# Kernel optimization log

Measured on AMD Instinct MI355X. Metric: run time of the kernel, lower is better.

Reference implementation:

```python
import jax, jax.numpy as jnp
import numpy as np

N = 50000
E = 800000


def _gcn_norm(edge_index, n):
    # Add self-loops and compute symmetric normalization coefficients per edge.
    src, dst = edge_index[0], edge_index[1]
    loop = jnp.arange(n, dtype=src.dtype)
    src = jnp.concatenate([src, loop])
    dst = jnp.concatenate([dst, loop])
    deg = jax.ops.segment_sum(jnp.ones_like(dst, dtype=jnp.float32), dst, num_segments=n)
    dis = jnp.where(deg > 0, 1.0 / jnp.sqrt(deg), 0.0)  # deg^-1/2
    norm = dis[src] * dis[dst]  # [E+N]
    return src, dst, norm


def _gcn_conv(x, W, b, src, dst, norm, n):
    h = x @ W                       # [N, F_out] dense transform first (PyG order)
    msg = h[src] * norm[:, None]    # gather + edgewise scale
    out = jax.ops.segment_sum(msg, dst, num_segments=n)  # scatter-add aggregate
    return out + b


def setup_inputs() -> dict:
    key = jax.random.key(0)
    ks = jax.random.split(key, 5)
    x = jax.random.normal(ks[0], (N, 128), dtype=jnp.float32)
    edge_index = jax.random.randint(ks[1], (2, E), 0, N, dtype=jnp.int64)
    s = 1.0 / np.sqrt(128.0)
    W1 = jax.random.normal(ks[2], (128, 128), dtype=jnp.float32) * s
    b1 = jnp.zeros((128,), dtype=jnp.float32)
    W_mu = jax.random.normal(ks[3], (128, 64), dtype=jnp.float32) * s
    b_mu = jnp.zeros((64,), dtype=jnp.float32)
    W_lv = jax.random.normal(ks[4], (128, 64), dtype=jnp.float32) * s
    b_lv = jnp.zeros((64,), dtype=jnp.float32)
    return {"x": x, "edge_index": edge_index, "W1": W1, "b1": b1,
            "W_mu": W_mu, "b_mu": b_mu, "W_lv": W_lv, "b_lv": b_lv}


def reference(x, edge_index, W1, b1, W_mu, b_mu, W_lv, b_lv):
    n = x.shape[0]
    src, dst, norm = _gcn_norm(edge_index, n)  # cached=True: same norm reused by all convs
    h = jax.nn.relu(_gcn_conv(x, W1, b1, src, dst, norm, n))
    mu = _gcn_conv(h, W_mu, b_mu, src, dst, norm, n)
    logvar = _gcn_conv(h, W_lv, b_lv, src, dst, norm, n)
    return mu, logvar
```

## Files before the change

kernel.cpp:

```cpp
#include <hip/hip_runtime.h>
#include <hip/hip_bf16.h>

#define THREADS 256
#define PCHUNK 8192
#define BN 512
#define BSH 9

typedef _Float16 half8 __attribute__((ext_vector_type(8)));
typedef float f32x4 __attribute__((ext_vector_type(4)));

__device__ __forceinline__ unsigned pack2(float a, float b) {
    __hip_bfloat16 ba = __float2bfloat16(a);
    __hip_bfloat16 bb = __float2bfloat16(b);
    unsigned short ua, ub;
    __builtin_memcpy(&ua, &ba, 2);
    __builtin_memcpy(&ub, &bb, 2);
    return ((unsigned)ub << 16) | ua;
}
__device__ __forceinline__ unsigned short bf16u(float a) {
    __hip_bfloat16 ba = __float2bfloat16(a);
    unsigned short ua;
    __builtin_memcpy(&ua, &ba, 2);
    return ua;
}
__device__ __forceinline__ float unpack_lo(unsigned u) { return __uint_as_float(u << 16); }
__device__ __forceinline__ float unpack_hi(unsigned u) { return __uint_as_float(u & 0xffff0000u); }


__global__ __launch_bounds__(256) void k_part_count(const int* __restrict__ dst,
                                                    int* __restrict__ cnt2,
                                                    int E, int nbuck, int numBlocks) {
    __shared__ int hist[128];
    for (int i = threadIdx.x; i < nbuck; i += 256) hist[i] = 0;
    __syncthreads();
    int base = blockIdx.x * PCHUNK;
    int cnt = min(PCHUNK, E - base);
    for (int i = threadIdx.x; i < cnt; i += 256)
        atomicAdd(&hist[dst[base + i] >> BSH], 1);
    __syncthreads();
    for (int b = threadIdx.x; b < nbuck; b += 256)
        cnt2[b * numBlocks + blockIdx.x] = hist[b];
}

__global__ __launch_bounds__(256) void k_scan_local(const int* __restrict__ count,
                                                    int* __restrict__ excl,
                                                    int* __restrict__ bsum, int n) {
    __shared__ int tile[256];
    int i = blockIdx.x * 256 + threadIdx.x;
    int v = (i < n) ? count[i] : 0;
    tile[threadIdx.x] = v;
    __syncthreads();
    for (int off = 1; off < 256; off <<= 1) {
        int add = (threadIdx.x >= off) ? tile[threadIdx.x - off] : 0;
        __syncthreads();
        tile[threadIdx.x] += add;
        __syncthreads();
    }
    if (i < n) excl[i] = tile[threadIdx.x] - v;
    if (threadIdx.x == 255) bsum[blockIdx.x] = tile[255];
}

__global__ __launch_bounds__(256) void k_scan_bsum(int* __restrict__ bsum, int nb) {
    __shared__ int tile[256];
    int v = (threadIdx.x < nb) ? bsum[threadIdx.x] : 0;
    tile[threadIdx.x] = v;
    __syncthreads();
    for (int off = 1; off < 256; off <<= 1) {
        int add = (threadIdx.x >= off) ? tile[threadIdx.x - off] : 0;
        __syncthreads();
        tile[threadIdx.x] += add;
        __syncthreads();
    }
    if (threadIdx.x < nb) bsum[threadIdx.x] = tile[threadIdx.x] - v;
}

__global__ void k_scan_add2(const int* __restrict__ excl, const int* __restrict__ bsum,
                            int* __restrict__ outv, int m) {
    int i = blockIdx.x * blockDim.x + threadIdx.x;
    if (i < m) outv[i] = excl[i] + bsum[i >> 8];
}

__global__ __launch_bounds__(256) void k_part_scatter(const int* __restrict__ src,
                                                      const int* __restrict__ dst,
                                                      const int* __restrict__ off,
                                                      int2* __restrict__ sorted,
                                                      int E, int nbuck, int numBlocks) {
    __shared__ int cur[128];
    for (int i = threadIdx.x; i < nbuck; i += 256)
        cur[i] = off[i * numBlocks + blockIdx.x];
    __syncthreads();
    int base = blockIdx.x * PCHUNK;
    int cnt = min(PCHUNK, E - base);
    for (int i = threadIdx.x; i < cnt; i += 256) {
        int d = dst[base + i];
        int s = src[base + i];
        int pos = atomicAdd(&cur[d >> BSH], 1);
        sorted[pos] = make_int2(s, d);
    }
}

__global__ __launch_bounds__(256) void k_bucket_build(const int2* __restrict__ sorted,
                                                      const int* __restrict__ off,
                                                      int* __restrict__ rowptr,
                                                      float* __restrict__ dis,
                                                      int* __restrict__ col,
                                                      int E, int n, int nbuck, int numBlocks) {
    __shared__ int hist[BN];
    __shared__ int scanv[BN];
    __shared__ int carry;
    const int b = blockIdx.x;
    const int lo = b << BSH;
    const int s = off[b * numBlocks];
    const int e = (b + 1 < nbuck) ? off[(b + 1) * numBlocks] : E;

    for (int i = threadIdx.x; i < BN; i += 256) hist[i] = 0;
    __syncthreads();
    for (int k = s + threadIdx.x; k < e; k += 256)
        atomicAdd(&hist[sorted[k].y - lo], 1);
    __syncthreads();

    if (threadIdx.x == 0) carry = 0;
    __syncthreads();
    for (int t = 0; t < BN / 256; ++t) {
        int i = t * 256 + threadIdx.x;
        int v = hist[i];
        scanv[i] = v;
        __syncthreads();
        for (int o = 1; o < 256; o <<= 1) {
            int add = (threadIdx.x >= o) ? scanv[t * 256 + threadIdx.x - o] : 0;
            __syncthreads();
            scanv[i] += add;
            __syncthreads();
        }
        int incl = scanv[i];
        scanv[i] = carry + incl - v;
        __syncthreads();
        if (threadIdx.x == 255) carry += incl;
        __syncthreads();
    }

    for (int i = threadIdx.x; i < BN; i += 256) {
        int node = lo + i;
        if (node < n) {
            rowptr[node] = s + scanv[i];
            dis[node] = rsqrtf((float)(hist[i] + 1));
        }
    }
    if (b == 0 && threadIdx.x == 0) rowptr[n] = E;
    __syncthreads();

    for (int k = s + threadIdx.x; k < e; k += 256) {
        int2 ed = sorted[k];
        int pos = s + atomicAdd(&scanv[ed.y - lo], 1);
        col[pos] = ed.x;
    }
}


__global__ __launch_bounds__(256) void k_gemm128_mfma(const float* __restrict__ A,
                                                      const float* __restrict__ W,
                                                      const float* __restrict__ dis,
                                                      unsigned short* __restrict__ outb,
                                                      int n) {
    __shared__ _Float16 Wl[16384];
    for (int slot = threadIdx.x; slot < 2048; slot += 256) {
        int l = slot & 63;
        int cs = slot >> 6;
        int s = cs & 3, c = cs >> 2;
        int colw = c * 16 + (l & 15);
        int k0 = s * 32 + (l >> 4) * 4;
        const float* wp0 = W + (size_t)k0 * 128 + colw;
        const float* wp1 = wp0 + 16 * 128;
        half8 h;
        h[0] = (_Float16)wp0[0];   h[1] = (_Float16)wp0[128];
        h[2] = (_Float16)wp0[256]; h[3] = (_Float16)wp0[384];
        h[4] = (_Float16)wp1[0];   h[5] = (_Float16)wp1[128];
        h[6] = (_Float16)wp1[256]; h[7] = (_Float16)wp1[384];
        *(half8*)(Wl + (size_t)slot * 8) = h;
    }
    __syncthreads();

    const int l  = threadIdx.x & 63;
    const int wid = threadIdx.x >> 6;
    const int lm = l & 15, q = l >> 4;
    const int rowA = blockIdx.x * 64 + wid * 16 + lm;
    const int ra = (rowA < n) ? rowA : (n - 1);

    f32x4 acc[8];
#pragma unroll
    for (int c = 0; c < 8; ++c) acc[c] = (f32x4){0.f, 0.f, 0.f, 0.f};

#pragma unroll
    for (int s = 0; s < 4; ++s) {
        const float* ap = A + (size_t)ra * 128 + s * 32 + q * 4;
        float4 a0 = *(const float4*)ap;
        float4 a1 = *(const float4*)(ap + 16);
        half8 af;
        af[0] = (_Float16)a0.x; af[1] = (_Float16)a0.y;
        af[2] = (_Float16)a0.z; af[3] = (_Float16)a0.w;
        af[4] = (_Float16)a1.x; af[5] = (_Float16)a1.y;
        af[6] = (_Float16)a1.z; af[7] = (_Float16)a1.w;
#pragma unroll
        for (int c = 0; c < 8; ++c) {
            half8 bf = *(half8*)(Wl + ((size_t)((c * 4 + s) * 64 + l)) * 8);
            acc[c] = __builtin_amdgcn_mfma_f32_16x16x32_f16(af, bf, acc[c], 0, 0, 0);
        }
    }

    const int gr0 = blockIdx.x * 64 + wid * 16 + q * 4;
#pragma unroll
    for (int r = 0; r < 4; ++r) {
        int gr = gr0 + r;
        if (gr >= n) continue;
        float dv = dis[gr];
#pragma unroll
        for (int c = 0; c < 8; ++c)
            outb[(size_t)gr * 128 + c * 16 + lm] = bf16u(acc[c][r] * dv);
    }
}


__global__ __launch_bounds__(256) void k_gemm_out_mfma(const float* __restrict__ A,
                                                       const float* __restrict__ Wmu,
                                                       const float* __restrict__ Wlv,
                                                       const float* __restrict__ bmu,
                                                       const float* __restrict__ blv,
                                                       float* __restrict__ out, int n) {
    __shared__ _Float16 Wl[16384];
    for (int slot = threadIdx.x; slot < 2048; slot += 256) {
        int l = slot & 63;
        int cs = slot >> 6;
        int s = cs & 3, c = cs >> 2;
        int colw = c * 16 + (l & 15);
        const float* Wsrc = (colw < 64) ? Wmu : Wlv;
        int cj = colw & 63;
        int k0 = s * 32 + (l >> 4) * 4;
        const float* wp0 = Wsrc + (size_t)k0 * 64 + cj;
        const float* wp1 = wp0 + 16 * 64;
        half8 h;
        h[0] = (_Float16)wp0[0];   h[1] = (_Float16)wp0[64];
        h[2] = (_Float16)wp0[128]; h[3] = (_Float16)wp0[192];
        h[4] = (_Float16)wp1[0];   h[5] = (_Float16)wp1[64];
        h[6] = (_Float16)wp1[128]; h[7] = (_Float16)wp1[192];
        *(half8*)(Wl + (size_t)slot * 8) = h;
    }
    __syncthreads();

    const int l  = threadIdx.x & 63;
    const int wid = threadIdx.x >> 6;
    const int lm = l & 15, q = l >> 4;
    const int rowA = blockIdx.x * 64 + wid * 16 + lm;
    const int ra = (rowA < n) ? rowA : (n - 1);

    f32x4 acc[8];
#pragma unroll
    for (int c = 0; c < 8; ++c) {
        int colw = c * 16 + lm;
        float bv = (colw < 64) ? bmu[colw] : blv[colw - 64];
        acc[c] = (f32x4){bv, bv, bv, bv};
    }

#pragma unroll
    for (int s = 0; s < 4; ++s) {
        const float* ap = A + (size_t)ra * 128 + s * 32 + q * 4;
        float4 a0 = *(const float4*)ap;
        float4 a1 = *(const float4*)(ap + 16);
        half8 af;
        af[0] = (_Float16)a0.x; af[1] = (_Float16)a0.y;
        af[2] = (_Float16)a0.z; af[3] = (_Float16)a0.w;
        af[4] = (_Float16)a1.x; af[5] = (_Float16)a1.y;
        af[6] = (_Float16)a1.z; af[7] = (_Float16)a1.w;
#pragma unroll
        for (int c = 0; c < 8; ++c) {
            half8 bf = *(half8*)(Wl + ((size_t)((c * 4 + s) * 64 + l)) * 8);
            acc[c] = __builtin_amdgcn_mfma_f32_16x16x32_f16(af, bf, acc[c], 0, 0, 0);
        }
    }

    float* lvp = out + (size_t)n * 64;
    const int gr0 = blockIdx.x * 64 + wid * 16 + q * 4;
#pragma unroll
    for (int r = 0; r < 4; ++r) {
        int gr = gr0 + r;
        if (gr >= n) continue;
#pragma unroll
        for (int c = 0; c < 8; ++c) {
            int colw = c * 16 + lm;
            float v = acc[c][r];
            if (colw < 64) out[(size_t)gr * 64 + colw] = v;
            else           lvp[(size_t)gr * 64 + (colw - 64)] = v;
        }
    }
}


template <bool PASS2>
__global__ __launch_bounds__(256) void k_agg(const uint4* __restrict__ hb,
                                             const int* __restrict__ rowptr,
                                             const int* __restrict__ col,
                                             const float* __restrict__ dis,
                                             const float* __restrict__ bias,
                                             uint4* __restrict__ outb,
                                             float* __restrict__ outf, int n) {
    int node = blockIdx.x * 4 + (threadIdx.x >> 6);
    if (node >= n) return;
    int lane = threadIdx.x & 63;
    int q = lane >> 4, l = lane & 15;
    float di = dis[node];

    float acc[8];
#pragma unroll
    for (int c = 0; c < 8; ++c) acc[c] = 0.f;

    int end = rowptr[node + 1];
    int k = rowptr[node] + q;

    uint4 v0 = {0, 0, 0, 0};
    int s1 = (k + 4 < end) ? col[k + 4] : -1;
    if (k < end) v0 = hb[(size_t)col[k] * 16 + l];

    while (k < end) {
        int s2 = (k + 8 < end) ? col[k + 8] : -1;
        uint4 v1 = {0, 0, 0, 0};
        if (s1 >= 0) v1 = hb[(size_t)s1 * 16 + l];

        acc[0] += unpack_lo(v0.x); acc[1] += unpack_hi(v0.x);
        acc[2] += unpack_lo(v0.y); acc[3] += unpack_hi(v0.y);
        acc[4] += unpack_lo(v0.z); acc[5] += unpack_hi(v0.z);
        acc[6] += unpack_lo(v0.w); acc[7] += unpack_hi(v0.w);

        v0 = v1; s1 = s2; k += 4;
    }

#pragma unroll
    for (int c = 0; c < 8; ++c) acc[c] += __shfl_xor(acc[c], 16);
#pragma unroll
    for (int c = 0; c < 8; ++c) acc[c] += __shfl_xor(acc[c], 32);

    if (q == 0) {
        uint4 sv = hb[(size_t)node * 16 + l];
        acc[0] += unpack_lo(sv.x); acc[1] += unpack_hi(sv.x);
        acc[2] += unpack_lo(sv.y); acc[3] += unpack_hi(sv.y);
        acc[4] += unpack_lo(sv.z); acc[5] += unpack_hi(sv.z);
        acc[6] += unpack_lo(sv.w); acc[7] += unpack_hi(sv.w);
        if (!PASS2) {
            float4 b0 = *(const float4*)(bias + l * 8);
            float4 b1 = *(const float4*)(bias + l * 8 + 4);
            float bv[8] = {b0.x, b0.y, b0.z, b0.w, b1.x, b1.y, b1.z, b1.w};
#pragma unroll
            for (int c = 0; c < 8; ++c)
                acc[c] = fmaxf(acc[c] * di + bv[c], 0.f) * di;
            uint4 o;
            o.x = pack2(acc[0], acc[1]);
            o.y = pack2(acc[2], acc[3]);
            o.z = pack2(acc[4], acc[5]);
            o.w = pack2(acc[6], acc[7]);
            outb[(size_t)node * 16 + l] = o;
        } else {
#pragma unroll
            for (int c = 0; c < 8; ++c) acc[c] *= di;
            float4 o0 = {acc[0], acc[1], acc[2], acc[3]};
            float4 o1 = {acc[4], acc[5], acc[6], acc[7]};
            *(float4*)(outf + (size_t)node * 128 + l * 8)     = o0;
            *(float4*)(outf + (size_t)node * 128 + l * 8 + 4) = o1;
        }
    }
}


extern "C" void kernel_launch(void* const* d_in, const int* in_sizes, int n_in,
                              void* d_out, int out_size, void* d_ws, size_t ws_size,
                              hipStream_t stream) {
    const float* x   = (const float*)d_in[0];
    const int*   ei  = (const int*)d_in[1];
    const float* W1  = (const float*)d_in[2];
    const float* b1  = (const float*)d_in[3];
    const float* Wmu = (const float*)d_in[4];
    const float* bmu = (const float*)d_in[5];
    const float* Wlv = (const float*)d_in[6];
    const float* blv = (const float*)d_in[7];
    float* out = (float*)d_out;

    const int n = in_sizes[0] / 128;
    const int E = in_sizes[1] / 2;
    const int* src = ei;
    const int* dst = ei + E;

    char* ws = (char*)d_ws;
    float* dis    = (float*)(ws + 0x00000);
    int*   rowptr = (int*)  (ws + 0x40000);
    int*   cnt2   = (int*)  (ws + 0x80000);
    int*   cnt2s  = (int*)  (ws + 0xC0000);
    int*   excl   = (int*)  (ws + 0x100000);
    int*   bsum   = (int*)  (ws + 0x140000);
    int*   col    = (int*)  (ws + 0x180000);
    uint4* h1b    = (uint4*)(ws + 0x580000);
    uint4* r1b    = (uint4*)(ws + 0x1200000);
    float* agg2   = (float*)(ws + 0x1E40000);
    int2*  sorted = (int2*) (ws + 0x1E40000);

    const int gAgg  = (n + 3) / 4;
    const int gGemm = (n + 63) / 64;
    const int nbuck   = (n + BN - 1) / BN;
    const int pBlocks = (E + PCHUNK - 1) / PCHUNK;
    const int m2      = nbuck * pBlocks;
    const int gM2     = (m2 + 255) / 256;

    k_part_count  <<<pBlocks, THREADS, 0, stream>>>(dst, cnt2, E, nbuck, pBlocks);
    k_scan_local  <<<gM2, THREADS, 0, stream>>>(cnt2, excl, bsum, m2);
    k_scan_bsum   <<<1, THREADS, 0, stream>>>(bsum, gM2);
    k_scan_add2   <<<gM2, THREADS, 0, stream>>>(excl, bsum, cnt2s, m2);
    k_part_scatter<<<pBlocks, THREADS, 0, stream>>>(src, dst, cnt2s, sorted, E, nbuck, pBlocks);
    k_bucket_build<<<nbuck, THREADS, 0, stream>>>(sorted, cnt2s, rowptr, dis, col, E, n, nbuck, pBlocks);

    k_gemm128_mfma<<<gGemm, THREADS, 0, stream>>>(x, W1, dis, (unsigned short*)h1b, n);

    k_agg<false><<<gAgg, THREADS, 0, stream>>>(h1b, rowptr, col, dis, b1, r1b, nullptr, n);

    k_agg<true><<<gAgg, THREADS, 0, stream>>>(r1b, rowptr, col, dis, nullptr, nullptr, agg2, n);

    k_gemm_out_mfma<<<gGemm, THREADS, 0, stream>>>(agg2, Wmu, Wlv, bmu, blv, out, n);
}
```

Measured before the change: 143.7 us.

## Pack sorted edges, fold scan add into consumers, store layer-2 aggregate as bf16

Drops the separate scan-add kernel: the scatter and bucket-build kernels now compute offsets from excl and bsum directly. Sorted edges are packed into one int (src shifted left, low bits the local dst), which halves that buffer's traffic. The second aggregation now writes bf16 instead of fp32, and the output GEMM reads it with bf16 MFMA, cutting write and read bytes. The cost is bf16 precision on the aggregate and fp16-to-bf16 weights, and the packing assumes src fits in 23 bits.

```diff
diff --git a/kernel.cpp b/kernel.cpp
--- a/kernel.cpp
+++ b/kernel.cpp
@@ -7,6 +7,7 @@
 #define BSH 9
 
 typedef _Float16 half8 __attribute__((ext_vector_type(8)));
+typedef short bf16x8 __attribute__((ext_vector_type(8)));
 typedef float f32x4 __attribute__((ext_vector_type(4)));
 
 __device__ __forceinline__ unsigned pack2(float a, float b) {
@@ -74,20 +75,19 @@
     if (threadIdx.x < nb) bsum[threadIdx.x] = tile[threadIdx.x] - v;
 }
 
-__global__ void k_scan_add2(const int* __restrict__ excl, const int* __restrict__ bsum,
-                            int* __restrict__ outv, int m) {
-    int i = blockIdx.x * blockDim.x + threadIdx.x;
-    if (i < m) outv[i] = excl[i] + bsum[i >> 8];
+__device__ __forceinline__ int scan_off(const int* excl, const int* bsum, int idx) {
+    return excl[idx] + bsum[idx >> 8];
 }
 
 __global__ __launch_bounds__(256) void k_part_scatter(const int* __restrict__ src,
                                                       const int* __restrict__ dst,
-                                                      const int* __restrict__ off,
-                                                      int2* __restrict__ sorted,
+                                                      const int* __restrict__ excl,
+                                                      const int* __restrict__ bsum,
+                                                      int* __restrict__ sorted,
                                                       int E, int nbuck, int numBlocks) {
     __shared__ int cur[128];
     for (int i = threadIdx.x; i < nbuck; i += 256)
-        cur[i] = off[i * numBlocks + blockIdx.x];
+        cur[i] = scan_off(excl, bsum, i * numBlocks + blockIdx.x);
     __syncthreads();
     int base = blockIdx.x * PCHUNK;
     int cnt = min(PCHUNK, E - base);
@@ -95,12 +95,13 @@
         int d = dst[base + i];
         int s = src[base + i];
         int pos = atomicAdd(&cur[d >> BSH], 1);
-        sorted[pos] = make_int2(s, d);
-    }
-}
-
-__global__ __launch_bounds__(256) void k_bucket_build(const int2* __restrict__ sorted,
-                                                      const int* __restrict__ off,
+        sorted[pos] = (s << BSH) | (d & (BN - 1));
+    }
+}
+
+__global__ __launch_bounds__(256) void k_bucket_build(const int* __restrict__ sorted,
+                                                      const int* __restrict__ excl,
+                                                      const int* __restrict__ bsum,
                                                       int* __restrict__ rowptr,
                                                       float* __restrict__ dis,
                                                       int* __restrict__ col,
@@ -110,13 +111,13 @@
     __shared__ int carry;
     const int b = blockIdx.x;
     const int lo = b << BSH;
-    const int s = off[b * numBlocks];
-    const int e = (b + 1 < nbuck) ? off[(b + 1) * numBlocks] : E;
+    const int s = scan_off(excl, bsum, b * numBlocks);
+    const int e = (b + 1 < nbuck) ? scan_off(excl, bsum, (b + 1) * numBlocks) : E;
 
     for (int i = threadIdx.x; i < BN; i += 256) hist[i] = 0;
     __syncthreads();
     for (int k = s + threadIdx.x; k < e; k += 256)
-        atomicAdd(&hist[sorted[k].y - lo], 1);
+        atomicAdd(&hist[sorted[k] & (BN - 1)], 1);
     __syncthreads();
 
     if (threadIdx.x == 0) carry = 0;
@@ -150,9 +151,9 @@
     __syncthreads();
 
     for (int k = s + threadIdx.x; k < e; k += 256) {
-        int2 ed = sorted[k];
-        int pos = s + atomicAdd(&scanv[ed.y - lo], 1);
-        col[pos] = ed.x;
+        int v = sorted[k];
+        int pos = s + atomicAdd(&scanv[v & (BN - 1)], 1);
+        col[pos] = ((unsigned)v) >> BSH;
     }
 }
 
@@ -220,13 +221,13 @@
 }
 
 
-__global__ __launch_bounds__(256) void k_gemm_out_mfma(const float* __restrict__ A,
+__global__ __launch_bounds__(256) void k_gemm_out_bf16(const unsigned short* __restrict__ Ab,
                                                        const float* __restrict__ Wmu,
                                                        const float* __restrict__ Wlv,
                                                        const float* __restrict__ bmu,
                                                        const float* __restrict__ blv,
                                                        float* __restrict__ out, int n) {
-    __shared__ _Float16 Wl[16384];
+    __shared__ unsigned short Wl[16384];
     for (int slot = threadIdx.x; slot < 2048; slot += 256) {
         int l = slot & 63;
         int cs = slot >> 6;
@@ -237,12 +238,12 @@
         int k0 = s * 32 + (l >> 4) * 4;
         const float* wp0 = Wsrc + (size_t)k0 * 64 + cj;
         const float* wp1 = wp0 + 16 * 64;
-        half8 h;
-        h[0] = (_Float16)wp0[0];   h[1] = (_Float16)wp0[64];
-        h[2] = (_Float16)wp0[128]; h[3] = (_Float16)wp0[192];
-        h[4] = (_Float16)wp1[0];   h[5] = (_Float16)wp1[64];
-        h[6] = (_Float16)wp1[128]; h[7] = (_Float16)wp1[192];
-        *(half8*)(Wl + (size_t)slot * 8) = h;
+        unsigned short h[8];
+        h[0] = bf16u(wp0[0]);   h[1] = bf16u(wp0[64]);
+        h[2] = bf16u(wp0[128]); h[3] = bf16u(wp0[192]);
+        h[4] = bf16u(wp1[0]);   h[5] = bf16u(wp1[64]);
+        h[6] = bf16u(wp1[128]); h[7] = bf16u(wp1[192]);
+        *(uint4*)(Wl + (size_t)slot * 8) = *(uint4*)h;
     }
     __syncthreads();
 
@@ -262,18 +263,16 @@
 
 #pragma unroll
     for (int s = 0; s < 4; ++s) {
-        const float* ap = A + (size_t)ra * 128 + s * 32 + q * 4;
-        float4 a0 = *(const float4*)ap;
-        float4 a1 = *(const float4*)(ap + 16);
-        half8 af;
-        af[0] = (_Float16)a0.x; af[1] = (_Float16)a0.y;
-        af[2] = (_Float16)a0.z; af[3] = (_Float16)a0.w;
-        af[4] = (_Float16)a1.x; af[5] = (_Float16)a1.y;
-        af[6] = (_Float16)a1.z; af[7] = (_Float16)a1.w;
+        const unsigned short* ap = Ab + (size_t)ra * 128 + s * 32 + q * 4;
+        uint2 a0 = *(const uint2*)ap;
+        uint2 a1 = *(const uint2*)(ap + 16);
+        bf16x8 af;
+        __builtin_memcpy(&af, &a0, 8);
+        __builtin_memcpy(((char*)&af) + 8, &a1, 8);
 #pragma unroll
         for (int c = 0; c < 8; ++c) {
-            half8 bf = *(half8*)(Wl + ((size_t)((c * 4 + s) * 64 + l)) * 8);
-            acc[c] = __builtin_amdgcn_mfma_f32_16x16x32_f16(af, bf, acc[c], 0, 0, 0);
+            bf16x8 bf = *(bf16x8*)(Wl + ((size_t)((c * 4 + s) * 64 + l)) * 8);
+            acc[c] = __builtin_amdgcn_mfma_f32_16x16x32_bf16(af, bf, acc[c], 0, 0, 0);
         }
     }
 
@@ -300,8 +299,7 @@
                                              const int* __restrict__ col,
                                              const float* __restrict__ dis,
                                              const float* __restrict__ bias,
-                                             uint4* __restrict__ outb,
-                                             float* __restrict__ outf, int n) {
+                                             uint4* __restrict__ outb, int n) {
     int node = blockIdx.x * 4 + (threadIdx.x >> 6);
     if (node >= n) return;
     int lane = threadIdx.x & 63;
@@ -350,20 +348,16 @@
 #pragma unroll
             for (int c = 0; c < 8; ++c)
                 acc[c] = fmaxf(acc[c] * di + bv[c], 0.f) * di;
-            uint4 o;
-            o.x = pack2(acc[0], acc[1]);
-            o.y = pack2(acc[2], acc[3]);
-            o.z = pack2(acc[4], acc[5]);
-            o.w = pack2(acc[6], acc[7]);
-            outb[(size_t)node * 16 + l] = o;
         } else {
 #pragma unroll
             for (int c = 0; c < 8; ++c) acc[c] *= di;
-            float4 o0 = {acc[0], acc[1], acc[2], acc[3]};
-            float4 o1 = {acc[4], acc[5], acc[6], acc[7]};
-            *(float4*)(outf + (size_t)node * 128 + l * 8)     = o0;
-            *(float4*)(outf + (size_t)node * 128 + l * 8 + 4) = o1;
-        }
+        }
+        uint4 o;
+        o.x = pack2(acc[0], acc[1]);
+        o.y = pack2(acc[2], acc[3]);
+        o.z = pack2(acc[4], acc[5]);
+        o.w = pack2(acc[6], acc[7]);
+        outb[(size_t)node * 16 + l] = o;
     }
 }
 
@@ -390,14 +384,13 @@
     float* dis    = (float*)(ws + 0x00000);
     int*   rowptr = (int*)  (ws + 0x40000);
     int*   cnt2   = (int*)  (ws + 0x80000);
-    int*   cnt2s  = (int*)  (ws + 0xC0000);
     int*   excl   = (int*)  (ws + 0x100000);
     int*   bsum   = (int*)  (ws + 0x140000);
     int*   col    = (int*)  (ws + 0x180000);
     uint4* h1b    = (uint4*)(ws + 0x580000);
     uint4* r1b    = (uint4*)(ws + 0x1200000);
-    float* agg2   = (float*)(ws + 0x1E40000);
-    int2*  sorted = (int2*) (ws + 0x1E40000);
+    uint4* agg2b  = h1b;
+    int*   sorted = (int*)  (ws + 0x1E40000);
 
     const int gAgg  = (n + 3) / 4;
     const int gGemm = (n + 63) / 64;
@@ -409,15 +402,15 @@
     k_part_count  <<<pBlocks, THREADS, 0, stream>>>(dst, cnt2, E, nbuck, pBlocks);
     k_scan_local  <<<gM2, THREADS, 0, stream>>>(cnt2, excl, bsum, m2);
     k_scan_bsum   <<<1, THREADS, 0, stream>>>(bsum, gM2);
-    k_scan_add2   <<<gM2, THREADS, 0, stream>>>(excl, bsum, cnt2s, m2);
-    k_part_scatter<<<pBlocks, THREADS, 0, stream>>>(src, dst, cnt2s, sorted, E, nbuck, pBlocks);
-    k_bucket_build<<<nbuck, THREADS, 0, stream>>>(sorted, cnt2s, rowptr, dis, col, E, n, nbuck, pBlocks);
+    k_part_scatter<<<pBlocks, THREADS, 0, stream>>>(src, dst, excl, bsum, sorted, E, nbuck, pBlocks);
+    k_bucket_build<<<nbuck, THREADS, 0, stream>>>(sorted, excl, bsum, rowptr, dis, col, E, n, nbuck, pBlocks);
 
     k_gemm128_mfma<<<gGemm, THREADS, 0, stream>>>(x, W1, dis, (unsigned short*)h1b, n);
 
-    k_agg<false><<<gAgg, THREADS, 0, stream>>>(h1b, rowptr, col, dis, b1, r1b, nullptr, n);
-
-    k_agg<true><<<gAgg, THREADS, 0, stream>>>(r1b, rowptr, col, dis, nullptr, nullptr, agg2, n);
-
-    k_gemm_out_mfma<<<gGemm, THREADS, 0, stream>>>(agg2, Wmu, Wlv, bmu, blv, out, n);
-}
+    k_agg<false><<<gAgg, THREADS, 0, stream>>>(h1b, rowptr, col, dis, b1, r1b, n);
+
+    k_agg<true><<<gAgg, THREADS, 0, stream>>>(r1b, rowptr, col, dis, nullptr, agg2b, n);
+
+    k_gemm_out_bf16<<<gGemm, THREADS, 0, stream>>>((const unsigned short*)agg2b,
+                                                   Wmu, Wlv, bmu, blv, out, n);
+}
```

Result: faster. 139.0 us (-3.3%).
